# Performance work log

Hardware: AMD Instinct MI355X
Metric: run time of the kernel (lower is better)

## Reference

```python
import jax, jax.numpy as jnp
import numpy as np

B, R, P = 2, 4096, 64
CD, CF, D, H, W = 1, 64, 16, 256, 256


def trilinear_sample(vol, pts):
    """F.grid_sample 3D, mode='bilinear', align_corners=True, padding_mode='zeros'.
    vol: [C,D,H,W]; pts: [N,3] normalized xyz coords in [-1,1] (x->W, y->H, z->D).
    Returns [N,C]. Interp weights computed once per point (fused gather)."""
    C, d, h, w = vol.shape
    x = (pts[:, 0] + 1.0) * 0.5 * (w - 1)
    y = (pts[:, 1] + 1.0) * 0.5 * (h - 1)
    z = (pts[:, 2] + 1.0) * 0.5 * (d - 1)
    x0 = jnp.floor(x); y0 = jnp.floor(y); z0 = jnp.floor(z)
    tx = x - x0; ty = y - y0; tz = z - z0
    x0i = x0.astype(jnp.int32); y0i = y0.astype(jnp.int32); z0i = z0.astype(jnp.int32)
    acc = jnp.zeros((pts.shape[0], C), dtype=vol.dtype)
    for dz in (0, 1):
        zi = z0i + dz
        wz = jnp.where(dz == 1, tz, 1.0 - tz)
        for dy in (0, 1):
            yi = y0i + dy
            wy = jnp.where(dy == 1, ty, 1.0 - ty)
            for dx in (0, 1):
                xi = x0i + dx
                wx = jnp.where(dx == 1, tx, 1.0 - tx)
                valid = ((xi >= 0) & (xi < w) & (yi >= 0) & (yi < h)
                         & (zi >= 0) & (zi < d))
                wgt = (wz * wy * wx * valid.astype(vol.dtype))  # zeros padding
                v = vol[:, jnp.clip(zi, 0, d - 1), jnp.clip(yi, 0, h - 1),
                        jnp.clip(xi, 0, w - 1)]  # [C,N]
                acc = acc + v.T * wgt[:, None]
    return acc


def setup_inputs() -> dict:
    key = jax.random.key(0)
    ks = jax.random.split(key, 6)
    density = jax.random.normal(ks[0], (B, CD, D, H, W), dtype=jnp.float32)
    features = jax.random.normal(ks[1], (B, CF, D, H, W), dtype=jnp.float32)
    # Row-vector-convention world->local transform (pytorch3d Transform3d):
    # near-identity so most sample points land inside the grid.
    w2l = (jnp.broadcast_to(jnp.eye(4, dtype=jnp.float32), (B, 4, 4))
           + 0.01 * jax.random.normal(ks[2], (B, 4, 4), dtype=jnp.float32))
    origins = jax.random.uniform(ks[3], (B, R, 3), dtype=jnp.float32,
                                 minval=-0.5, maxval=0.5)
    dirs = jax.random.normal(ks[4], (B, R, 3), dtype=jnp.float32)
    directions = dirs / jnp.linalg.norm(dirs, axis=-1, keepdims=True)
    lengths = jnp.sort(jax.random.uniform(ks[5], (B, R, P), dtype=jnp.float32,
                                          minval=0.0, maxval=1.5), axis=-1)
    return {"density": density, "features": features, "world_to_local": w2l,
            "origins": origins, "directions": directions, "lengths": lengths}


def reference(density, features, world_to_local, origins, directions, lengths):
    M = world_to_local  # [B,4,4], p_local = [p,1] @ M (w column is e4, no divide)
    o_loc = jnp.einsum('bri,bij->brj', origins, M[:, :3, :3]) + M[:, 3:4, :3]
    d_loc = jnp.einsum('bri,bij->brj', directions, M[:, :3, :3])
    pts = o_loc[:, :, None, :] + d_loc[:, :, None, :] * lengths[..., None]  # [B,R,P,3]
    vol = jnp.concatenate([density, features], axis=1)  # fuse: weights computed once
    samp = jax.vmap(trilinear_sample)(vol, pts.reshape(pts.shape[0], -1, 3))
    samp = samp.reshape(pts.shape[0], pts.shape[1], pts.shape[2], -1)
    cd = density.shape[1]
    return samp[..., :cd], samp[..., cd:]
```

## Files before the change

kernel.cpp:

```cpp
#include <hip/hip_runtime.h>
#include <cstdint>
#include <cstddef>

constexpr int kB  = 2;
constexpr int kR  = 4096;
constexpr int kP  = 64;
constexpr int kCF = 64;
constexpr int kD  = 16;
constexpr int kH  = 256;
constexpr int kW  = 256;
constexpr int kHW = kH * kW;
constexpr size_t kDHW = (size_t)kD * kHW;

struct Corners { int vox[8]; float w[8]; };

__device__ __forceinline__ Corners make_corners(float px, float py, float pz) {
    const float fx = (px + 1.0f) * 0.5f * (float)(kW - 1);
    const float fy = (py + 1.0f) * 0.5f * (float)(kH - 1);
    const float fz = (pz + 1.0f) * 0.5f * (float)(kD - 1);
    const float x0f = floorf(fx), y0f = floorf(fy), z0f = floorf(fz);
    const float tx = fx - x0f, ty = fy - y0f, tz = fz - z0f;
    const int x0 = (int)x0f, y0 = (int)y0f, z0 = (int)z0f;

    const float wxv[2] = {1.0f - tx, tx};
    const float wyv[2] = {1.0f - ty, ty};
    const float wzv[2] = {1.0f - tz, tz};
    const int xs[2] = {x0, x0 + 1};
    const int ys[2] = {y0, y0 + 1};
    const int zs[2] = {z0, z0 + 1};

    Corners c;
    #pragma unroll
    for (int iz = 0; iz < 2; ++iz) {
        const int zi = zs[iz];
        const bool vz = (zi >= 0) & (zi < kD);
        const int zb = min(max(zi, 0), kD - 1) * kHW;
        #pragma unroll
        for (int iy = 0; iy < 2; ++iy) {
            const int yi = ys[iy];
            const bool vy = (yi >= 0) & (yi < kH);
            const int zyb = zb + min(max(yi, 0), kH - 1) * kW;
            const float wzy = wzv[iz] * wyv[iy];
            #pragma unroll
            for (int ix = 0; ix < 2; ++ix) {
                const int xi = xs[ix];
                const bool vx = (xi >= 0) & (xi < kW);
                const int k = iz * 4 + iy * 2 + ix;
                c.vox[k] = zyb + min(max(xi, 0), kW - 1);
                c.w[k]   = wzy * wxv[ix] * ((vz & vy & vx) ? 1.0f : 0.0f);
            }
        }
    }
    return c;
}

__global__ __launch_bounds__(256) void transpose_cf(
    const float* __restrict__ features,
    float* __restrict__ ftr)
{
    __shared__ float tile[64][65];
    const int bid = blockIdx.x;
    const int xt  = bid & 3;
    const int y   = (bid >> 2) & 255;
    const int z   = (bid >> 10) & 15;
    const int b   = bid >> 14;
    const int x0  = xt * 64;
    const int t   = threadIdx.x;
    const int sub = (t & 15) * 4;
    const int rr  = t >> 4;

    const size_t rbase = (size_t)b * 64 * kDHW + (size_t)z * kHW + (size_t)y * kW + x0;
    #pragma unroll
    for (int i = 0; i < 4; ++i) {
        const int c = rr + 16 * i;
        const float4 v = *(const float4*)(features + rbase + (size_t)c * kDHW + sub);
        tile[c][sub + 0] = v.x; tile[c][sub + 1] = v.y;
        tile[c][sub + 2] = v.z; tile[c][sub + 3] = v.w;
    }
    __syncthreads();

    float* dst0 = ftr + (((size_t)(b * kD + z) * kH + y) * kW + x0) * 64;
    #pragma unroll
    for (int i = 0; i < 4; ++i) {
        const int x = rr + 16 * i;
        float4 v;
        v.x = tile[sub + 0][x]; v.y = tile[sub + 1][x];
        v.z = tile[sub + 2][x]; v.w = tile[sub + 3][x];
        *(float4*)(dst0 + (size_t)x * 64 + sub) = v;
    }
}

__global__ __launch_bounds__(256) void sample_tr(
    const float* __restrict__ density,
    const float* __restrict__ ftr,
    const float* __restrict__ w2l,
    const float* __restrict__ origins,
    const float* __restrict__ dirs,
    const float* __restrict__ lengths,
    float* __restrict__ out_d,
    float* __restrict__ out_f)
{
    const int lane = threadIdx.x & 63;
    const int wv   = threadIdx.x >> 6;
    const int ray  = blockIdx.x * 4 + wv;
    const int b    = ray >> 12;

    const float* M   = w2l + (size_t)b * 16;
    const float* org = origins + (size_t)ray * 3;
    const float* dir = dirs    + (size_t)ray * 3;
    const float ox = org[0], oy = org[1], oz = org[2];
    const float dx = dir[0], dy = dir[1], dz = dir[2];

    const float olx = ox*M[0] + oy*M[4] + oz*M[8]  + M[12];
    const float oly = ox*M[1] + oy*M[5] + oz*M[9]  + M[13];
    const float olz = ox*M[2] + oy*M[6] + oz*M[10] + M[14];
    const float dlx = dx*M[0] + dy*M[4] + dz*M[8];
    const float dly = dx*M[1] + dy*M[5] + dz*M[9];
    const float dlz = dx*M[2] + dy*M[6] + dz*M[10];

    const float* db = density + (size_t)b * kDHW;
    const float tlen = lengths[(size_t)ray * kP + lane];

    {
        const float t  = tlen;
        const Corners c = make_corners(olx + dlx * t, oly + dly * t, olz + dlz * t);
        float accd = 0.0f;
        #pragma unroll
        for (int k = 0; k < 8; ++k)
            if (c.w[k] != 0.0f) accd += c.w[k] * db[c.vox[k]];
        out_d[(size_t)ray * kP + lane] = accd;
    }

    const int grp = lane >> 4;
    const int c4  = (lane & 15) * 4;
    const float* fb = ftr + (size_t)b * kDHW * 64 + c4;
    float* ofr = out_f + (size_t)ray * kP * 64 + c4;

    for (int pg = 0; pg < kP / 4; ++pg) {
        const int p = pg * 4 + grp;
        const float t  = __shfl(tlen, p);
        const Corners c = make_corners(olx + dlx * t, oly + dly * t, olz + dlz * t);
        float4 acc = {0.f, 0.f, 0.f, 0.f};
        #pragma unroll
        for (int k = 0; k < 8; ++k) {
            const float w = c.w[k];
            if (w != 0.0f) {
                const float4 v = *(const float4*)(fb + (size_t)c.vox[k] * 64);
                acc.x += w * v.x; acc.y += w * v.y;
                acc.z += w * v.z; acc.w += w * v.w;
            }
        }
        *(float4*)(ofr + (size_t)p * 64) = acc;
    }
}

__global__ __launch_bounds__(256) void grid_sampler_direct(
    const float* __restrict__ density,
    const float* __restrict__ features,
    const float* __restrict__ w2l,
    const float* __restrict__ origins,
    const float* __restrict__ dirs,
    const float* __restrict__ lengths,
    float* __restrict__ out_d,
    float* __restrict__ out_f)
{
    const int lane = threadIdx.x & 63;
    const int wv   = threadIdx.x >> 6;
    const int ray  = blockIdx.x * 4 + wv;
    const int b    = ray >> 12;

    const float* M   = w2l + (size_t)b * 16;
    const float* org = origins + (size_t)ray * 3;
    const float* dir = dirs    + (size_t)ray * 3;
    const float ox = org[0], oy = org[1], oz = org[2];
    const float dx = dir[0], dy = dir[1], dz = dir[2];

    const float olx = ox*M[0] + oy*M[4] + oz*M[8]  + M[12];
    const float oly = ox*M[1] + oy*M[5] + oz*M[9]  + M[13];
    const float olz = ox*M[2] + oy*M[6] + oz*M[10] + M[14];
    const float dlx = dx*M[0] + dy*M[4] + dz*M[8];
    const float dly = dx*M[1] + dy*M[5] + dz*M[9];
    const float dlz = dx*M[2] + dy*M[6] + dz*M[10];

    const float* fb = features + (size_t)b * kCF * kDHW + (size_t)lane * kDHW;
    const float* db = density  + (size_t)b * kDHW;
    const float tlen = lengths[(size_t)ray * kP + lane];

    {
        const float t  = tlen;
        const Corners c = make_corners(olx + dlx * t, oly + dly * t, olz + dlz * t);
        float accd = 0.0f;
        #pragma unroll
        for (int k = 0; k < 8; ++k)
            if (c.w[k] != 0.0f) accd += c.w[k] * db[c.vox[k]];
        out_d[(size_t)ray * kP + lane] = accd;
    }

    float* ofr = out_f + (size_t)ray * kP * 64 + lane;
    for (int p = 0; p < kP; ++p) {
        const float t  = __shfl(tlen, p);
        const Corners c = make_corners(olx + dlx * t, oly + dly * t, olz + dlz * t);
        float acc = 0.0f;
        #pragma unroll
        for (int k = 0; k < 8; ++k)
            if (c.w[k] != 0.0f) acc += c.w[k] * fb[c.vox[k]];
        ofr[(size_t)p * 64] = acc;
    }
}

extern "C" void kernel_launch(void* const* d_in, const int* in_sizes, int n_in,
                              void* d_out, int out_size, void* d_ws, size_t ws_size,
                              hipStream_t stream) {
    const float* density  = (const float*)d_in[0];
    const float* features = (const float*)d_in[1];
    const float* w2l      = (const float*)d_in[2];
    const float* origins  = (const float*)d_in[3];
    const float* dirs     = (const float*)d_in[4];
    const float* lengths  = (const float*)d_in[5];

    float* out_d = (float*)d_out;
    float* out_f = out_d + (size_t)kB * kR * kP;

    const size_t need = (size_t)kB * kDHW * 64 * sizeof(float);

    if (ws_size >= need) {
        float* ftr = (float*)d_ws;
        hipLaunchKernelGGL(transpose_cf, dim3(kB * kD * kH * (kW / 64)), dim3(256),
                           0, stream, features, ftr);
        hipLaunchKernelGGL(sample_tr, dim3(kB * kR / 4), dim3(256), 0, stream,
                           density, ftr, w2l, origins, dirs, lengths, out_d, out_f);
    } else {
        hipLaunchKernelGGL(grid_sampler_direct, dim3(kB * kR / 4), dim3(256), 0, stream,
                           density, features, w2l, origins, dirs, lengths, out_d, out_f);
    }
}
```

Before: 926.4 us.

## Store transposed features as fp16 and add wave-uniform in-bounds fast path

```diff
diff --git a/kernel.cpp b/kernel.cpp
--- a/kernel.cpp
+++ b/kernel.cpp
@@ -1,4 +1,5 @@
 #include <hip/hip_runtime.h>
+#include <hip/hip_fp16.h>
 #include <cstdint>
 #include <cstddef>
 
@@ -12,7 +13,10 @@
 constexpr int kHW = kH * kW;
 constexpr size_t kDHW = (size_t)kD * kHW;
 
-struct Corners { int vox[8]; float w[8]; };
+typedef float    v4f __attribute__((ext_vector_type(4)));
+typedef uint32_t v4u __attribute__((ext_vector_type(4)));
+
+struct Corners { int vox[8]; float w[8]; int status; };
 
 __device__ __forceinline__ Corners make_corners(float px, float py, float pz) {
     const float fx = (px + 1.0f) * 0.5f * (float)(kW - 1);
@@ -51,12 +55,17 @@
             }
         }
     }
+    const bool allIn  = (x0 >= 0) & (x0 <= kW - 2) & (y0 >= 0) & (y0 <= kH - 2)
+                      & (z0 >= 0) & (z0 <= kD - 2);
+    const bool allOut = (x0 < -1) | (x0 > kW - 1) | (y0 < -1) | (y0 > kH - 1)
+                      | (z0 < -1) | (z0 > kD - 1);
+    c.status = allIn ? 2 : (allOut ? 0 : 1);
     return c;
 }
 
 __global__ __launch_bounds__(256) void transpose_cf(
     const float* __restrict__ features,
-    float* __restrict__ ftr)
+    __half* __restrict__ ftr)
 {
     __shared__ float tile[64][65];
     const int bid = blockIdx.x;
@@ -73,26 +82,27 @@
     #pragma unroll
     for (int i = 0; i < 4; ++i) {
         const int c = rr + 16 * i;
-        const float4 v = *(const float4*)(features + rbase + (size_t)c * kDHW + sub);
+        const v4f v = __builtin_nontemporal_load(
+            (const v4f*)(features + rbase + (size_t)c * kDHW + sub));
         tile[c][sub + 0] = v.x; tile[c][sub + 1] = v.y;
         tile[c][sub + 2] = v.z; tile[c][sub + 3] = v.w;
     }
     __syncthreads();
 
-    float* dst0 = ftr + (((size_t)(b * kD + z) * kH + y) * kW + x0) * 64;
+    const size_t voxbase = (((size_t)(b * kD + z) * kH + y) * kW + x0);
     #pragma unroll
     for (int i = 0; i < 4; ++i) {
         const int x = rr + 16 * i;
-        float4 v;
-        v.x = tile[sub + 0][x]; v.y = tile[sub + 1][x];
-        v.z = tile[sub + 2][x]; v.w = tile[sub + 3][x];
-        *(float4*)(dst0 + (size_t)x * 64 + sub) = v;
+        union { __half2 h[2]; uint2 u; } pk;
+        pk.h[0] = __floats2half2_rn(tile[sub + 0][x], tile[sub + 1][x]);
+        pk.h[1] = __floats2half2_rn(tile[sub + 2][x], tile[sub + 3][x]);
+        *(uint2*)(ftr + (voxbase + x) * 64 + sub) = pk.u;
     }
 }
 
 __global__ __launch_bounds__(256) void sample_tr(
     const float* __restrict__ density,
-    const float* __restrict__ ftr,
+    const __half* __restrict__ ftr,
     const float* __restrict__ w2l,
     const float* __restrict__ origins,
     const float* __restrict__ dirs,
@@ -125,32 +135,58 @@
         const float t  = tlen;
         const Corners c = make_corners(olx + dlx * t, oly + dly * t, olz + dlz * t);
         float accd = 0.0f;
-        #pragma unroll
-        for (int k = 0; k < 8; ++k)
-            if (c.w[k] != 0.0f) accd += c.w[k] * db[c.vox[k]];
-        out_d[(size_t)ray * kP + lane] = accd;
-    }
-
-    const int grp = lane >> 4;
-    const int c4  = (lane & 15) * 4;
-    const float* fb = ftr + (size_t)b * kDHW * 64 + c4;
-    float* ofr = out_f + (size_t)ray * kP * 64 + c4;
-
-    for (int pg = 0; pg < kP / 4; ++pg) {
-        const int p = pg * 4 + grp;
+        if (c.status != 0) {
+            #pragma unroll
+            for (int k = 0; k < 8; ++k)
+                if (c.w[k] != 0.0f) accd += c.w[k] * db[c.vox[k]];
+        }
+        __builtin_nontemporal_store(accd, out_d + (size_t)ray * kP + lane);
+    }
+
+    const int grp = lane >> 3;
+    const int c8  = (lane & 7) * 8;
+    const __half* fb = ftr + (size_t)b * kDHW * 64 + c8;
+    float* ofr = out_f + (size_t)ray * kP * 64 + c8;
+
+    for (int pg = 0; pg < kP / 8; ++pg) {
+        const int p = pg * 8 + grp;
         const float t  = __shfl(tlen, p);
         const Corners c = make_corners(olx + dlx * t, oly + dly * t, olz + dlz * t);
-        float4 acc = {0.f, 0.f, 0.f, 0.f};
-        #pragma unroll
-        for (int k = 0; k < 8; ++k) {
-            const float w = c.w[k];
-            if (w != 0.0f) {
-                const float4 v = *(const float4*)(fb + (size_t)c.vox[k] * 64);
-                acc.x += w * v.x; acc.y += w * v.y;
-                acc.z += w * v.z; acc.w += w * v.w;
+        float a0=0.f,a1=0.f,a2=0.f,a3=0.f,a4=0.f,a5=0.f,a6=0.f,a7=0.f;
+
+        if (__all(c.status == 2)) {
+            #pragma unroll
+            for (int k = 0; k < 8; ++k) {
+                union { v4u u; __half2 h[4]; } U;
+                U.u = *(const v4u*)(fb + (size_t)c.vox[k] * 64);
+                const float w = c.w[k];
+                const float2 f0 = __half22float2(U.h[0]);
+                const float2 f1 = __half22float2(U.h[1]);
+                const float2 f2 = __half22float2(U.h[2]);
+                const float2 f3 = __half22float2(U.h[3]);
+                a0 += w * f0.x; a1 += w * f0.y; a2 += w * f1.x; a3 += w * f1.y;
+                a4 += w * f2.x; a5 += w * f2.y; a6 += w * f3.x; a7 += w * f3.y;
             }
-        }
-        *(float4*)(ofr + (size_t)p * 64) = acc;
+        } else if (!__all(c.status == 0)) {
+            #pragma unroll
+            for (int k = 0; k < 8; ++k) {
+                const float w = c.w[k];
+                if (w != 0.0f) {
+                    union { v4u u; __half2 h[4]; } U;
+                    U.u = *(const v4u*)(fb + (size_t)c.vox[k] * 64);
+                    const float2 f0 = __half22float2(U.h[0]);
+                    const float2 f1 = __half22float2(U.h[1]);
+                    const float2 f2 = __half22float2(U.h[2]);
+                    const float2 f3 = __half22float2(U.h[3]);
+                    a0 += w * f0.x; a1 += w * f0.y; a2 += w * f1.x; a3 += w * f1.y;
+                    a4 += w * f2.x; a5 += w * f2.y; a6 += w * f3.x; a7 += w * f3.y;
+                }
+            }
+        }
+        v4f s0; s0.x = a0; s0.y = a1; s0.z = a2; s0.w = a3;
+        v4f s1; s1.x = a4; s1.y = a5; s1.z = a6; s1.w = a7;
+        __builtin_nontemporal_store(s0, (v4f*)(ofr + (size_t)p * 64));
+        __builtin_nontemporal_store(s1, (v4f*)(ofr + (size_t)p * 64 + 4));
     }
 }
 
@@ -190,9 +226,11 @@
         const float t  = tlen;
         const Corners c = make_corners(olx + dlx * t, oly + dly * t, olz + dlz * t);
         float accd = 0.0f;
-        #pragma unroll
-        for (int k = 0; k < 8; ++k)
-            if (c.w[k] != 0.0f) accd += c.w[k] * db[c.vox[k]];
+        if (c.status != 0) {
+            #pragma unroll
+            for (int k = 0; k < 8; ++k)
+                if (c.w[k] != 0.0f) accd += c.w[k] * db[c.vox[k]];
+        }
         out_d[(size_t)ray * kP + lane] = accd;
     }
 
@@ -201,9 +239,11 @@
         const float t  = __shfl(tlen, p);
         const Corners c = make_corners(olx + dlx * t, oly + dly * t, olz + dlz * t);
         float acc = 0.0f;
-        #pragma unroll
-        for (int k = 0; k < 8; ++k)
-            if (c.w[k] != 0.0f) acc += c.w[k] * fb[c.vox[k]];
+        if (c.status != 0) {
+            #pragma unroll
+            for (int k = 0; k < 8; ++k)
+                if (c.w[k] != 0.0f) acc += c.w[k] * fb[c.vox[k]];
+        }
         ofr[(size_t)p * 64] = acc;
     }
 }
@@ -221,10 +261,10 @@
     float* out_d = (float*)d_out;
     float* out_f = out_d + (size_t)kB * kR * kP;
 
-    const size_t need = (size_t)kB * kDHW * 64 * sizeof(float);
+    const size_t need = (size_t)kB * kDHW * 64 * sizeof(__half);
 
     if (ws_size >= need) {
-        float* ftr = (float*)d_ws;
+        __half* ftr = (__half*)d_ws;
         hipLaunchKernelGGL(transpose_cf, dim3(kB * kD * kH * (kW / 64)), dim3(256),
                            0, stream, features, ftr);
         hipLaunchKernelGGL(sample_tr, dim3(kB * kR / 4), dim3(256), 0, stream,
```

Result: faster. 812.5 us (-12.3%).
